# Optimization experiments

Measured on AMD Instinct MI355X. Metric: run time of the kernel, lower is better.

Reference implementation:

```python
import jax, jax.numpy as jnp
import numpy as np

D_STATE = 16
D_CONV = 4


def rmsnorm(x, w, eps=1e-6):
    # normalize over last (channel) axis
    return x * jax.lax.rsqrt(jnp.mean(x * x, axis=-1, keepdims=True) + eps) * w


def silu(x):
    return x * jax.nn.sigmoid(x)


def mamba(x, in_proj_w, conv1d_w, conv1d_b, x_proj_w, dt_proj_w, dt_proj_b, A_log, D_param, out_proj_w):
    # x: [B, L, C], d_inner == C (expand=1)
    B, L, C = x.shape
    dt_rank = dt_proj_w.shape[1]
    xz = jnp.einsum('blc,ec->ble', x, in_proj_w)  # [B, L, 2C]
    u, z = jnp.split(xz, 2, axis=-1)
    # causal depthwise conv1d over time (pad left d_conv-1)
    uc = jax.lax.conv_general_dilated(
        u.transpose(0, 2, 1), conv1d_w[:, None, :], (1,), [(D_CONV - 1, 0)],
        dimension_numbers=('NCH', 'OIH', 'NCH'), feature_group_count=C)
    u = silu((uc + conv1d_b[None, :, None]).transpose(0, 2, 1))  # [B, L, C]
    x_dbl = jnp.einsum('blc,ec->ble', u, x_proj_w)  # [B, L, dt_rank + 2*N]
    dt, Bm, Cm = jnp.split(x_dbl, [dt_rank, dt_rank + D_STATE], axis=-1)
    delta = jax.nn.softplus(jnp.einsum('blr,dr->bld', dt, dt_proj_w) + dt_proj_b)  # [B, L, C]
    A = -jnp.exp(A_log)  # [C, N]
    deltaA = jnp.exp(delta[..., None] * A)              # [B, L, C, N]
    deltaBu = (delta * u)[..., None] * Bm[:, :, None, :]  # [B, L, C, N]

    def step(h, inp):
        dA, dBu, c = inp
        h = dA * h + dBu
        return h, jnp.einsum('bdn,bn->bd', h, c)

    h0 = jnp.zeros((B, C, D_STATE), x.dtype)
    _, ys = jax.lax.scan(step, h0, (deltaA.transpose(1, 0, 2, 3),
                                    deltaBu.transpose(1, 0, 2, 3),
                                    Cm.transpose(1, 0, 2)))
    y = ys.transpose(1, 0, 2) + u * D_param  # [B, L, C]
    y = y * silu(z)
    return jnp.einsum('bld,od->blo', y, out_proj_w)


def reference(x, norm_w, in_proj_w, conv1d_w, conv1d_b, x_proj_w, dt_proj_w, dt_proj_b,
              A_log, D_param, out_proj_w, scale_mod, dw_w, dw_b, res_scale):
    B, C, H, W = x.shape
    x_cl = x.transpose(0, 2, 3, 1)              # [B, H, W, C]
    xn_cl = rmsnorm(x_cl, norm_w)
    x_norm = xn_cl.transpose(0, 3, 1, 2)        # [B, C, H, W]
    # bidirectional Mamba over flattened spatial sequence
    x_flat = xn_cl.reshape(B, H * W, C)
    mparams = (in_proj_w, conv1d_w, conv1d_b, x_proj_w, dt_proj_w, dt_proj_b, A_log, D_param, out_proj_w)
    fwd = mamba(x_flat, *mparams)
    bwd = jnp.flip(mamba(jnp.flip(x_flat, axis=1), *mparams), axis=1)
    g = (fwd + bwd) * scale_mod
    global_feat = g.reshape(B, H, W, C).transpose(0, 3, 1, 2)
    # local spatial gating: sigmoid(depthwise 3x3 conv) * x_norm
    conv = jax.lax.conv_general_dilated(
        x_norm, dw_w[:, None, :, :], (1, 1), [(1, 1), (1, 1)],
        dimension_numbers=('NCHW', 'OIHW', 'NCHW'), feature_group_count=C)
    local_feat = jax.nn.sigmoid(conv + dw_b[None, :, None, None]) * x_norm
    return x + res_scale * (global_feat + local_feat)


def setup_inputs() -> dict:
    key = jax.random.key(0)
    ks = jax.random.split(key, 10)
    B, C, H, W = 8, 384, 32, 32
    dt_rank = 24  # ceil(384 / 16)
    s = 0.02
    f32 = jnp.float32
    return {
        'x': jax.random.normal(ks[0], (B, C, H, W), f32),
        'norm_w': jnp.ones((C,), f32),
        'in_proj_w': jax.random.normal(ks[1], (2 * C, C), f32) * s,
        'conv1d_w': jax.random.normal(ks[2], (C, D_CONV), f32) * 0.2,
        'conv1d_b': jnp.zeros((C,), f32),
        'x_proj_w': jax.random.normal(ks[3], (dt_rank + 2 * D_STATE, C), f32) * s,
        'dt_proj_w': jax.random.normal(ks[4], (C, dt_rank), f32) * 0.1,
        'dt_proj_b': jax.random.uniform(ks[5], (C,), f32, -4.0, -2.0),
        'A_log': jnp.log(jnp.tile(jnp.arange(1, D_STATE + 1, dtype=f32), (C, 1))),
        'D_param': jnp.ones((C,), f32),
        'out_proj_w': jax.random.normal(ks[6], (C, C), f32) * s,
        'scale_mod': jnp.full((1,), 0.25, f32),
        'dw_w': jax.random.normal(ks[7], (C, 3, 3), f32) * 0.1,
        'dw_b': jnp.zeros((C,), f32),
        'res_scale': jnp.full((1,), 0.5, f32),
    }
```

## Files before the change

kernel.cpp:

```cpp
#include <hip/hip_runtime.h>
#include <hip/hip_bf16.h>


typedef __attribute__((ext_vector_type(8))) short bf16x8;
typedef __attribute__((ext_vector_type(8))) unsigned short u16x8;
typedef __attribute__((ext_vector_type(4))) float f32x4;

#define L2E 1.44269504088896340736f

static __device__ __forceinline__ unsigned short f2bf(float f) {
  unsigned int u = __builtin_bit_cast(unsigned int, f);
  u += 0x7fff + ((u >> 16) & 1);
  return (unsigned short)(u >> 16);
}
static __device__ __forceinline__ float bf2f(unsigned short u) {
  unsigned int v = (unsigned int)u << 16;
  return __builtin_bit_cast(float, v);
}

#define GLOAD_LDS16(g, l)                                             \
  __builtin_amdgcn_global_load_lds(                                   \
      (const __attribute__((address_space(1))) unsigned int*)(g),     \
      (__attribute__((address_space(3))) unsigned int*)(l), 16, 0, 0)

__global__ __launch_bounds__(256) void prep_k(
    const float* __restrict__ in_w, const float* __restrict__ x_w,
    const float* __restrict__ dt_w, const float* __restrict__ out_w,
    const float* __restrict__ A_log, const float* __restrict__ nw,
    unsigned short* __restrict__ W_in, unsigned short* __restrict__ W_out,
    unsigned short* __restrict__ Wcomb, float* __restrict__ A2) {
  int idx = blockIdx.x * 256 + threadIdx.x;
  switch (blockIdx.y) {
    case 0: if (idx < 768 * 384) W_in[idx] = f2bf(in_w[idx] * nw[idx % 384]); break;
    case 1: if (idx < 384 * 384) W_out[idx] = f2bf(out_w[idx]); break;
    case 2: if (idx < 384 * 16) A2[idx] = -expf(A_log[idx]) * L2E; break;
    case 3: if (idx < 384 * 384) {
        int o = idx / 384, c = idx - o * 384;
        float s = 0.f;
        #pragma unroll
        for (int r = 0; r < 24; ++r) s += dt_w[o * 24 + r] * x_w[r * 384 + c];
        Wcomb[idx] = f2bf(s);
      } break;
    case 4: if (idx < 128 * 384) {
        int n = idx / 384, k = idx - n * 384;
        Wcomb[147456 + idx] = f2bf(n < 32 ? x_w[(24 + n) * 384 + k] : 0.f);
      } break;
  }
}

__global__ __launch_bounds__(256) void transpose_k(
    const float* __restrict__ x, unsigned short* __restrict__ xb,
    float* __restrict__ nf) {
  const int b = blockIdx.y;
  const int l0 = blockIdx.x * 32;
  const int tid = threadIdx.x;
  const int cr = tid >> 5, lw = tid & 31;
  const int cj = tid & 63, lr = tid >> 6;
  __shared__ float t64[64][33];
  __shared__ float part[8][33];
  float acc = 0.f;
  for (int cc = 0; cc < 6; ++cc) {
    #pragma unroll
    for (int k = 0; k < 8; ++k) {
      int cp = k * 8 + cr;
      int c = cc * 64 + cp;
      float v = x[(((size_t)(b * 384 + c)) << 10) + l0 + lw];
      t64[cp][lw] = v;
      acc = fmaf(v, v, acc);
    }
    __syncthreads();
    #pragma unroll
    for (int k2 = 0; k2 < 8; ++k2) {
      int ll = lr + 4 * k2;
      xb[((size_t)((b << 10) + l0 + ll)) * 384 + cc * 64 + cj] = f2bf(t64[cj][ll]);
    }
    __syncthreads();
  }
  part[cr][lw] = acc;
  __syncthreads();
  if (tid < 32) {
    float s = part[0][tid] + part[1][tid] + part[2][tid] + part[3][tid] +
              part[4][tid] + part[5][tid] + part[6][tid] + part[7][tid];
    nf[(b << 10) + l0 + tid] = rsqrtf(s * (1.f / 384.f) + 1e-6f);
  }
}

template <int EPI, int SUMIN>
__global__ __launch_bounds__(256) void gemm128_k(
    const unsigned short* __restrict__ A0u, const unsigned short* __restrict__ A1u,
    const unsigned short* __restrict__ Bw, int K, int N,
    unsigned short* __restrict__ ob0, unsigned short* __restrict__ ob1,
    float* __restrict__ of0, float* __restrict__ of1,
    const float* __restrict__ aux) {
  const unsigned short* Au = (EPI == 2 && blockIdx.z) ? A1u : A0u;
  unsigned short* ob = (EPI == 2 && blockIdx.z) ? ob1 : ob0;
  float* of = (EPI == 2 && blockIdx.z) ? of1 : of0;
  __shared__ __attribute__((aligned(16))) unsigned short As[128 * 32];
  __shared__ __attribute__((aligned(16))) unsigned short Bs[128 * 32];
  const int n0 = blockIdx.x * 128, m0 = blockIdx.y * 128;
  const int tid = threadIdx.x;
  const int lane = tid & 63, wave = tid >> 6;
  const int wm = wave >> 1, wn = wave & 1;
  const int fr = lane & 15, ks = (lane >> 4) * 8;
  const int row = tid >> 2, colseg = (tid & 3) * 8;
  const unsigned short* pA0 = Au + (size_t)(m0 + row) * K + colseg;
  const unsigned short* pA1 = Au + (size_t)(m0 + 64 + row) * K + colseg;
  const unsigned short* pB0 = Bw + (size_t)(n0 + row) * K + colseg;
  const unsigned short* pB1 = Bw + (size_t)(n0 + 64 + row) * K + colseg;
  unsigned short* lA0 = As + wave * 512;
  unsigned short* lA1 = As + 2048 + wave * 512;
  unsigned short* lB0 = Bs + wave * 512;
  unsigned short* lB1 = Bs + 2048 + wave * 512;
  f32x4 acc[4][4] = {};
  for (int k0 = 0; k0 < K; k0 += 32) {
    __syncthreads();
    if (SUMIN) {
      #pragma unroll
      for (int p = 0; p < 2; ++p) {
        int r = p * 64 + row;
        u16x8 va = *(const u16x8*)&A0u[(size_t)(m0 + r) * K + k0 + colseg];
        u16x8 vb = *(const u16x8*)&A1u[(size_t)(m0 + r) * K + k0 + colseg];
        u16x8 s;
        #pragma unroll
        for (int j = 0; j < 8; ++j) s[j] = f2bf(bf2f(va[j]) + bf2f(vb[j]));
        *(u16x8*)&As[r * 32 + colseg] = s;
      }
    } else {
      GLOAD_LDS16(pA0, lA0);
      GLOAD_LDS16(pA1, lA1);
      pA0 += 32; pA1 += 32;
    }
    GLOAD_LDS16(pB0, lB0);
    GLOAD_LDS16(pB1, lB1);
    pB0 += 32; pB1 += 32;
    __syncthreads();
    bf16x8 af[4], bfr[4];
    #pragma unroll
    for (int mi = 0; mi < 4; ++mi)
      af[mi] = *(const bf16x8*)&As[(wm * 64 + mi * 16 + fr) * 32 + ks];
    #pragma unroll
    for (int ni = 0; ni < 4; ++ni)
      bfr[ni] = *(const bf16x8*)&Bs[(wn * 64 + ni * 16 + fr) * 32 + ks];
    #pragma unroll
    for (int mi = 0; mi < 4; ++mi)
      #pragma unroll
      for (int ni = 0; ni < 4; ++ni)
        acc[mi][ni] = __builtin_amdgcn_mfma_f32_16x16x32_bf16(af[mi], bfr[ni], acc[mi][ni], 0, 0, 0);
  }
  #pragma unroll
  for (int mi = 0; mi < 4; ++mi)
    #pragma unroll
    for (int ni = 0; ni < 4; ++ni)
      #pragma unroll
      for (int j = 0; j < 4; ++j) {
        int m = m0 + wm * 64 + mi * 16 + (lane >> 4) * 4 + j;
        int n = n0 + wn * 64 + ni * 16 + fr;
        float v = acc[mi][ni][j];
        if (EPI == 0) {
          ob0[(size_t)m * N + n] = f2bf(v * aux[m]);
        } else if (EPI == 2) {
          if (n < 384) {
            float t = v + aux[n];
            float sp = (t > 20.f) ? t : log1pf(expf(t));
            ob[(size_t)m * 384 + n] = f2bf(sp);
          } else if (n < 416) {
            of[(size_t)m * 32 + (n - 384)] = v;
          }
        } else {
          ob0[(size_t)m * N + n] = f2bf(v * aux[0]);
        }
      }
}

__global__ __launch_bounds__(384) void conv_silu_k(
    const unsigned short* __restrict__ xz, const float* __restrict__ cw,
    const float* __restrict__ cb,
    unsigned short* __restrict__ ub0, unsigned short* __restrict__ ub1) {
  const int st = blockIdx.x, b = blockIdx.y, dir = blockIdx.z;
  const int c = threadIdx.x;
  const int s0 = st * 8;
  const float w0 = cw[c * 4 + 0], w1 = cw[c * 4 + 1];
  const float w2 = cw[c * 4 + 2], w3 = cw[c * 4 + 3];
  const float bb = cb[c];
  unsigned short* ub = dir ? ub1 : ub0;
  float xv[11];
  #pragma unroll
  for (int k = 0; k < 11; ++k) {
    int j = s0 - 3 + k;
    float v = 0.f;
    if (j >= 0) {
      int t = dir ? (1023 - j) : j;
      v = bf2f(xz[(size_t)((b << 10) + t) * 768 + c]);
    }
    xv[k] = v;
  }
  #pragma unroll
  for (int s = 0; s < 8; ++s) {
    float a = bb + xv[s] * w0 + xv[s + 1] * w1 + xv[s + 2] * w2 + xv[s + 3] * w3;
    float uv = a * __builtin_amdgcn_rcpf(1.f + __builtin_amdgcn_exp2f(-a * L2E));
    ub[(size_t)((b << 10) + s0 + s) * 384 + c] = f2bf(uv);
  }
}

__global__ __launch_bounds__(512) void scan1_k(
    const unsigned short* __restrict__ de0, const unsigned short* __restrict__ de1,
    const unsigned short* __restrict__ ub0, const unsigned short* __restrict__ ub1,
    const float* __restrict__ bc0, const float* __restrict__ bc1,
    const float* __restrict__ A2, float* __restrict__ PH) {
  const int ct = blockIdx.x, b = blockIdx.y;
  const int dir = blockIdx.z >> 4, seg = blockIdx.z & 15;
  const unsigned short* del = dir ? de1 : de0;
  const unsigned short* uu  = dir ? ub1 : ub0;
  const float* bc  = dir ? bc1 : bc0;
  const int tid = threadIdx.x;
  const int lane = tid & 63, wave = tid >> 6;
  const int n = lane & 15, cg = lane >> 4;
  const int cl = wave * 4 + cg;
  const int c = ct * 32 + cl;
  const float a2 = A2[c * 16 + n];
  const size_t base = ((size_t)b << 10) + seg * 64;
  __shared__ __attribute__((aligned(16))) float sd[32][68];
  __shared__ __attribute__((aligned(16))) float su[32][68];
  __shared__ __attribute__((aligned(16))) float sB[16][68];
  const int li = tid >> 5, lj = tid & 31;
  const int li3 = tid >> 4, lj3 = tid & 15;
  unsigned short rd[4], ru[4];
  float rb[2];
  #pragma unroll
  for (int k = 0; k < 4; ++k) {
    size_t rowi = base + k * 16 + li;
    rd[k] = del[rowi * 384 + ct * 32 + lj];
    ru[k] = uu [rowi * 384 + ct * 32 + lj];
  }
  #pragma unroll
  for (int k = 0; k < 2; ++k)
    rb[k] = bc[(base + k * 32 + li3) * 32 + lj3];
  #pragma unroll
  for (int k = 0; k < 4; ++k) {
    float dd = bf2f(rd[k]);
    sd[lj][k * 16 + li] = dd;
    su[lj][k * 16 + li] = dd * bf2f(ru[k]);
  }
  #pragma unroll
  for (int k = 0; k < 2; ++k) sB[lj3][k * 32 + li3] = rb[k];
  __syncthreads();
  float h = 0.f, P = 1.f;
  for (int ch = 0; ch < 4; ++ch) {
    f32x4 dv[4], duv[4], bmv[4];
    #pragma unroll
    for (int r = 0; r < 4; ++r) {
      dv[r]  = *(const f32x4*)&sd[cl][ch * 16 + r * 4];
      duv[r] = *(const f32x4*)&su[cl][ch * 16 + r * 4];
      bmv[r] = *(const f32x4*)&sB[n][ch * 16 + r * 4];
    }
    #pragma unroll
    for (int i = 0; i < 16; ++i) {
      float dA = __builtin_amdgcn_exp2f(dv[i >> 2][i & 3] * a2);
      h = fmaf(dA, h, duv[i >> 2][i & 3] * bmv[i >> 2][i & 3]);
      P *= dA;
    }
  }
  size_t o = (size_t)((dir * 8 + b) * 16 + seg) * 6144 + c * 16 + n;
  *(float2*)&PH[o * 2] = make_float2(P, h);
}

__global__ __launch_bounds__(512) void scan2_k(
    const unsigned short* __restrict__ de0, const unsigned short* __restrict__ de1,
    const unsigned short* __restrict__ ub0, const unsigned short* __restrict__ ub1,
    const float* __restrict__ bc0, const float* __restrict__ bc1,
    const unsigned short* __restrict__ xz, const float* __restrict__ A2,
    const float* __restrict__ Dp, const float* __restrict__ PH,
    unsigned short* __restrict__ Sb0, unsigned short* __restrict__ Sb1) {
  const int ct = blockIdx.x, b = blockIdx.y;
  const int dir = blockIdx.z >> 4, seg = blockIdx.z & 15;
  const unsigned short* del = dir ? de1 : de0;
  const unsigned short* uu  = dir ? ub1 : ub0;
  const float* bc  = dir ? bc1 : bc0;
  unsigned short* S = dir ? Sb1 : Sb0;
  const int tid = threadIdx.x;
  const int lane = tid & 63, wave = tid >> 6;
  const int n = lane & 15, cg = lane >> 4;
  const int cl = wave * 4 + cg;
  const int c = ct * 32 + cl;
  const float a2 = A2[c * 16 + n];
  const float dpc = Dp[c];
  const size_t bb_ = (size_t)b << 10;
  const int segoff = seg * 64;
  __shared__ __attribute__((aligned(16))) float sd[32][68];
  __shared__ __attribute__((aligned(16))) float su[32][68];
  __shared__ __attribute__((aligned(16))) float sz[32][68];
  __shared__ __attribute__((aligned(16))) float sbc[32][68];
  __shared__ __attribute__((aligned(16))) unsigned short sy[64 * 36];
  const int li = tid >> 5, lj = tid & 31;
  unsigned short rd[4], ru[4], rz[4];
  float rb[4];
  #pragma unroll
  for (int k = 0; k < 4; ++k) {
    size_t rowi = bb_ + segoff + k * 16 + li;
    rd[k] = del[rowi * 384 + ct * 32 + lj];
    ru[k] = uu [rowi * 384 + ct * 32 + lj];
    int tz = dir ? (1023 - (segoff + k * 16 + li)) : (segoff + k * 16 + li);
    rz[k] = xz[(bb_ + tz) * 768 + 384 + ct * 32 + lj];
    rb[k] = bc[rowi * 32 + lj];
  }
  float h = 0.f;
  {
    size_t rb2 = (((size_t)(dir * 8 + b) * 16) * 6144 + c * 16 + n) * 2;
    #pragma unroll
    for (int s = 0; s < 15; ++s) {
      float2 ph = *(const float2*)&PH[rb2 + (size_t)s * 12288];
      h = (s < seg) ? fmaf(ph.x, h, ph.y) : h;
    }
  }
  #pragma unroll
  for (int k = 0; k < 4; ++k) {
    sd[lj][k * 16 + li] = bf2f(rd[k]);
    su[lj][k * 16 + li] = bf2f(ru[k]);
    sz[lj][k * 16 + li] = bf2f(rz[k]);
    sbc[lj][k * 16 + li] = rb[k];
  }
  __syncthreads();
  for (int ch = 0; ch < 4; ++ch) {
    f32x4 dv[4], uv4[4], bmv[4], cmv[4];
    #pragma unroll
    for (int r = 0; r < 4; ++r) {
      dv[r]  = *(const f32x4*)&sd[cl][ch * 16 + r * 4];
      uv4[r] = *(const f32x4*)&su[cl][ch * 16 + r * 4];
      bmv[r] = *(const f32x4*)&sbc[n][ch * 16 + r * 4];
      cmv[r] = *(const f32x4*)&sbc[16 + n][ch * 16 + r * 4];
    }
    float p[16];
    #pragma unroll
    for (int i = 0; i < 16; ++i) {
      float dd = dv[i >> 2][i & 3];
      float dA = __builtin_amdgcn_exp2f(dd * a2);
      h = fmaf(dA, h, dd * uv4[i >> 2][i & 3] * bmv[i >> 2][i & 3]);
      p[i] = h * cmv[i >> 2][i & 3];
    }
    float q8[8];
    #pragma unroll
    for (int j = 0; j < 8; ++j) {
      float send = (n & 8) ? p[j] : p[j + 8];
      float recv = __shfl_xor(send, 8);
      float keep = (n & 8) ? p[j + 8] : p[j];
      q8[j] = keep + recv;
    }
    float q4[4];
    #pragma unroll
    for (int j = 0; j < 4; ++j) {
      float send = (n & 4) ? q8[j] : q8[j + 4];
      float recv = __shfl_xor(send, 4);
      float keep = (n & 4) ? q8[j + 4] : q8[j];
      q4[j] = keep + recv;
    }
    float q2[2];
    #pragma unroll
    for (int j = 0; j < 2; ++j) {
      float send = (n & 2) ? q4[j] : q4[j + 2];
      float recv = __shfl_xor(send, 2);
      float keep = (n & 2) ? q4[j + 2] : q4[j];
      q2[j] = keep + recv;
    }
    float send = (n & 1) ? q2[0] : q2[1];
    float recv = __shfl_xor(send, 1);
    float keep = (n & 1) ? q2[1] : q2[0];
    float ysum = keep + recv;
    float uvn = su[cl][ch * 16 + n];
    float zz  = sz[cl][ch * 16 + n];
    float sig = __builtin_amdgcn_rcpf(1.f + __builtin_amdgcn_exp2f(-zz * L2E));
    float y = (ysum + uvn * dpc) * (zz * sig);
    sy[(ch * 16 + n) * 36 + cl] = f2bf(y);
  }
  __syncthreads();
  {
    const int t = tid >> 3, cq = (tid & 7) * 4;
    int tg = segoff + t;
    int trow = dir ? (1023 - tg) : tg;
    *(ushort4*)&S[(bb_ + trow) * 384 + ct * 32 + cq] =
        *(const ushort4*)&sy[t * 36 + cq];
  }
}

__global__ __launch_bounds__(256) void final_k(
    const unsigned short* __restrict__ Gb, const unsigned short* __restrict__ xb,
    const float* __restrict__ nf, const float* __restrict__ nw,
    const float* __restrict__ x, const float* __restrict__ dww,
    const float* __restrict__ dwb, const float* __restrict__ rs,
    float* __restrict__ out) {
  __shared__ float tile[64][33];
  __shared__ float wq[9][64];
  __shared__ float bbs[64], nws[64];
  const int l0 = blockIdx.x * 32, c0 = blockIdx.y * 64, b = blockIdx.z;
  const int tid = threadIdx.x;
  for (int i = tid; i < 576; i += 256) {
    int c = i / 9, q = i - c * 9;
    wq[q][c] = dww[(size_t)(c0 + c) * 9 + q] * nw[c0 + c];
  }
  if (tid < 64) { bbs[tid] = dwb[c0 + tid]; nws[tid] = nw[c0 + tid]; }
  __syncthreads();
  {
    const int oct = tid & 7, li = tid >> 3;
    const int l = l0 + li;
    const int hh = l >> 5, ww = l & 31;
    float acc[8];
    {
      f32x4 ba = *(const f32x4*)&bbs[oct * 8];
      f32x4 bb2 = *(const f32x4*)&bbs[oct * 8 + 4];
      #pragma unroll
      for (int j = 0; j < 4; ++j) { acc[j] = ba[j]; acc[j + 4] = bb2[j]; }
    }
    #pragma unroll
    for (int di = -1; di <= 1; ++di) {
      int h2 = hh + di;
      if (h2 < 0 || h2 > 31) continue;
      #pragma unroll
      for (int dj = -1; dj <= 1; ++dj) {
        int w2 = ww + dj;
        if (w2 < 0 || w2 > 31) continue;
        int lp = h2 * 32 + w2;
        float nfl = nf[(b << 10) + lp];
        u16x8 v = *(const u16x8*)&xb[(size_t)((b << 10) + lp) * 384 + c0 + oct * 8];
        int q = (di + 1) * 3 + (dj + 1);
        f32x4 wa = *(const f32x4*)&wq[q][oct * 8];
        f32x4 wb = *(const f32x4*)&wq[q][oct * 8 + 4];
        #pragma unroll
        for (int j = 0; j < 4; ++j) {
          acc[j]     = fmaf(bf2f(v[j]) * nfl, wa[j], acc[j]);
          acc[j + 4] = fmaf(bf2f(v[j + 4]) * nfl, wb[j], acc[j + 4]);
        }
      }
    }
    size_t ri = (size_t)((b << 10) + l) * 384 + c0 + oct * 8;
    float nfl0 = nf[(b << 10) + l];
    u16x8 xc = *(const u16x8*)&xb[ri];
    u16x8 gv = *(const u16x8*)&Gb[ri];
    #pragma unroll
    for (int j = 0; j < 8; ++j) {
      float xv = bf2f(xc[j]) * nfl0 * nws[oct * 8 + j];
      float sig = __builtin_amdgcn_rcpf(1.f + __builtin_amdgcn_exp2f(-acc[j] * L2E));
      tile[oct * 8 + j][li] = bf2f(gv[j]) + xv * sig;
    }
  }
  __syncthreads();
  {
    const int lw = tid & 31, cr = tid >> 5;
    const float rsv = rs[0];
    for (int p = 0; p < 8; ++p) {
      int c = c0 + p * 8 + cr;
      size_t o = ((size_t)(b * 384 + c) << 10) + l0 + lw;
      out[o] = x[o] + rsv * tile[p * 8 + cr][lw];
    }
  }
}

extern "C" void kernel_launch(void* const* d_in, const int* in_sizes, int n_in,
                              void* d_out, int out_size, void* d_ws, size_t ws_size,
                              hipStream_t stream) {
  const float* x         = (const float*)d_in[0];
  const float* norm_w    = (const float*)d_in[1];
  const float* in_proj_w = (const float*)d_in[2];
  const float* conv1d_w  = (const float*)d_in[3];
  const float* conv1d_b  = (const float*)d_in[4];
  const float* x_proj_w  = (const float*)d_in[5];
  const float* dt_proj_w = (const float*)d_in[6];
  const float* dt_proj_b = (const float*)d_in[7];
  const float* A_log     = (const float*)d_in[8];
  const float* D_param   = (const float*)d_in[9];
  const float* out_proj_w= (const float*)d_in[10];
  const float* scale_mod = (const float*)d_in[11];
  const float* dw_w      = (const float*)d_in[12];
  const float* dw_b      = (const float*)d_in[13];
  const float* res_scale = (const float*)d_in[14];
  float* out = (float*)d_out;

  char* base = (char*)d_ws;
  size_t off = 0;
  auto alloc = [&](size_t bytes) {
    off = (off + 255) & ~(size_t)255;
    void* p = base + off;
    off += bytes;
    return p;
  };
  const size_t B_BLC = (size_t)8192 * 384 * 2;

  unsigned short* xb   = (unsigned short*)alloc(B_BLC);
  float*          nf   = (float*)alloc((size_t)8192 * 4);
  unsigned short* xz   = (unsigned short*)alloc((size_t)8192 * 768 * 2);
  unsigned short* u_b0 = (unsigned short*)alloc(B_BLC);
  unsigned short* u_b1 = (unsigned short*)alloc(B_BLC);
  float*          bc0  = (float*)alloc((size_t)8192 * 32 * 4);
  float*          bc1  = (float*)alloc((size_t)8192 * 32 * 4);
  unsigned short* de0  = (unsigned short*)alloc(B_BLC);
  unsigned short* de1  = (unsigned short*)alloc(B_BLC);
  unsigned short* Sb0  = (unsigned short*)alloc(B_BLC);
  unsigned short* Sb1  = (unsigned short*)alloc(B_BLC);
  float*          PH   = (float*)alloc((size_t)1572864 * 2 * 4);
  unsigned short* W_in = (unsigned short*)alloc((size_t)768 * 384 * 2);
  unsigned short* W_out= (unsigned short*)alloc((size_t)384 * 384 * 2);
  unsigned short* Wcomb= (unsigned short*)alloc((size_t)512 * 384 * 2);
  float*          A2   = (float*)alloc((size_t)384 * 16 * 4);
  unsigned short* Gb   = (unsigned short*)alloc(B_BLC);

  prep_k<<<dim3(1152, 5), 256, 0, stream>>>(in_proj_w, x_proj_w, dt_proj_w,
                                            out_proj_w, A_log, norm_w,
                                            W_in, W_out, Wcomb, A2);
  transpose_k<<<dim3(32, 8), 256, 0, stream>>>(x, xb, nf);
  gemm128_k<0, 0><<<dim3(6, 64), 256, 0, stream>>>(xb, xb, W_in, 384, 768,
                                                   xz, xz, nullptr, nullptr, nf);
  conv_silu_k<<<dim3(128, 8, 2), 384, 0, stream>>>(xz, conv1d_w, conv1d_b,
                                                   u_b0, u_b1);
  gemm128_k<2, 0><<<dim3(4, 64, 2), 256, 0, stream>>>(u_b0, u_b1, Wcomb, 384, 512,
                                                      de0, de1, bc0, bc1,
                                                      dt_proj_b);
  scan1_k<<<dim3(12, 8, 32), 512, 0, stream>>>(de0, de1, u_b0, u_b1, bc0, bc1,
                                               A2, PH);
  scan2_k<<<dim3(12, 8, 32), 512, 0, stream>>>(de0, de1, u_b0, u_b1, bc0, bc1,
                                               xz, A2, D_param, PH, Sb0, Sb1);
  gemm128_k<3, 1><<<dim3(3, 64), 256, 0, stream>>>(Sb0, Sb1, W_out, 384, 384,
                                                   Gb, Gb, nullptr, nullptr,
                                                   scale_mod);
  final_k<<<dim3(32, 6, 8), 256, 0, stream>>>(Gb, xb, nf, norm_w, x, dw_w, dw_b,
                                              res_scale, out);
}
```

Measured before the change: 263.4 us.

## Replace 128x128 GEMM tiles with 64x64 tiles using register-prefetched padded LDS

New measurement: 245.4 us. -6.8%, faster.

```diff
diff --git a/kernel.cpp b/kernel.cpp
--- a/kernel.cpp
+++ b/kernel.cpp
@@ -17,11 +17,6 @@
   unsigned int v = (unsigned int)u << 16;
   return __builtin_bit_cast(float, v);
 }
-
-#define GLOAD_LDS16(g, l)                                             \
-  __builtin_amdgcn_global_load_lds(                                   \
-      (const __attribute__((address_space(1))) unsigned int*)(g),     \
-      (__attribute__((address_space(3))) unsigned int*)(l), 16, 0, 0)
 
 __global__ __launch_bounds__(256) void prep_k(
     const float* __restrict__ in_w, const float* __restrict__ x_w,
@@ -86,75 +81,65 @@
 }
 
 template <int EPI, int SUMIN>
-__global__ __launch_bounds__(256) void gemm128_k(
+__global__ __launch_bounds__(256) void gemm64_k(
     const unsigned short* __restrict__ A0u, const unsigned short* __restrict__ A1u,
     const unsigned short* __restrict__ Bw, int K, int N,
     unsigned short* __restrict__ ob0, unsigned short* __restrict__ ob1,
     float* __restrict__ of0, float* __restrict__ of1,
     const float* __restrict__ aux) {
-  const unsigned short* Au = (EPI == 2 && blockIdx.z) ? A1u : A0u;
-  unsigned short* ob = (EPI == 2 && blockIdx.z) ? ob1 : ob0;
-  float* of = (EPI == 2 && blockIdx.z) ? of1 : of0;
-  __shared__ __attribute__((aligned(16))) unsigned short As[128 * 32];
-  __shared__ __attribute__((aligned(16))) unsigned short Bs[128 * 32];
-  const int n0 = blockIdx.x * 128, m0 = blockIdx.y * 128;
+  const unsigned short* Au = blockIdx.z ? A1u : A0u;
+  unsigned short* ob = blockIdx.z ? ob1 : ob0;
+  float* of = blockIdx.z ? of1 : of0;
+  __shared__ unsigned short As[64][40];
+  __shared__ unsigned short Bs[64][40];
+  const int n0 = blockIdx.x * 64, m0 = blockIdx.y * 64;
   const int tid = threadIdx.x;
   const int lane = tid & 63, wave = tid >> 6;
   const int wm = wave >> 1, wn = wave & 1;
+  const int lrow = tid >> 2, lseg = (tid & 3) * 8;
   const int fr = lane & 15, ks = (lane >> 4) * 8;
-  const int row = tid >> 2, colseg = (tid & 3) * 8;
-  const unsigned short* pA0 = Au + (size_t)(m0 + row) * K + colseg;
-  const unsigned short* pA1 = Au + (size_t)(m0 + 64 + row) * K + colseg;
-  const unsigned short* pB0 = Bw + (size_t)(n0 + row) * K + colseg;
-  const unsigned short* pB1 = Bw + (size_t)(n0 + 64 + row) * K + colseg;
-  unsigned short* lA0 = As + wave * 512;
-  unsigned short* lA1 = As + 2048 + wave * 512;
-  unsigned short* lB0 = Bs + wave * 512;
-  unsigned short* lB1 = Bs + 2048 + wave * 512;
-  f32x4 acc[4][4] = {};
+  const unsigned short* pA = Au + (size_t)(m0 + lrow) * K + lseg;
+  const unsigned short* pA1 = A1u + (size_t)(m0 + lrow) * K + lseg;
+  const unsigned short* pB = Bw + (size_t)(n0 + lrow) * K + lseg;
+  u16x8 rva, rvb, rbb;
+  auto issue = [&](int k0) {
+    rva = *(const u16x8*)(pA + k0);
+    if (SUMIN) rvb = *(const u16x8*)(pA1 + k0);
+    rbb = *(const u16x8*)(pB + k0);
+  };
+  auto commit = [&]() {
+    u16x8 s = rva;
+    if (SUMIN) {
+      #pragma unroll
+      for (int j = 0; j < 8; ++j) s[j] = f2bf(bf2f(rva[j]) + bf2f(rvb[j]));
+    }
+    *(u16x8*)&As[lrow][lseg] = s;
+    *(u16x8*)&Bs[lrow][lseg] = rbb;
+  };
+  issue(0);
+  f32x4 acc[2][2] = {};
   for (int k0 = 0; k0 < K; k0 += 32) {
     __syncthreads();
-    if (SUMIN) {
-      #pragma unroll
-      for (int p = 0; p < 2; ++p) {
-        int r = p * 64 + row;
-        u16x8 va = *(const u16x8*)&A0u[(size_t)(m0 + r) * K + k0 + colseg];
-        u16x8 vb = *(const u16x8*)&A1u[(size_t)(m0 + r) * K + k0 + colseg];
-        u16x8 s;
-        #pragma unroll
-        for (int j = 0; j < 8; ++j) s[j] = f2bf(bf2f(va[j]) + bf2f(vb[j]));
-        *(u16x8*)&As[r * 32 + colseg] = s;
-      }
-    } else {
-      GLOAD_LDS16(pA0, lA0);
-      GLOAD_LDS16(pA1, lA1);
-      pA0 += 32; pA1 += 32;
-    }
-    GLOAD_LDS16(pB0, lB0);
-    GLOAD_LDS16(pB1, lB1);
-    pB0 += 32; pB1 += 32;
+    commit();
     __syncthreads();
-    bf16x8 af[4], bfr[4];
-    #pragma unroll
-    for (int mi = 0; mi < 4; ++mi)
-      af[mi] = *(const bf16x8*)&As[(wm * 64 + mi * 16 + fr) * 32 + ks];
-    #pragma unroll
-    for (int ni = 0; ni < 4; ++ni)
-      bfr[ni] = *(const bf16x8*)&Bs[(wn * 64 + ni * 16 + fr) * 32 + ks];
-    #pragma unroll
-    for (int mi = 0; mi < 4; ++mi)
-      #pragma unroll
-      for (int ni = 0; ni < 4; ++ni)
-        acc[mi][ni] = __builtin_amdgcn_mfma_f32_16x16x32_bf16(af[mi], bfr[ni], acc[mi][ni], 0, 0, 0);
-  }
-  #pragma unroll
-  for (int mi = 0; mi < 4; ++mi)
-    #pragma unroll
-    for (int ni = 0; ni < 4; ++ni)
+    if (k0 + 32 < K) issue(k0 + 32);
+    bf16x8 a0 = *(const bf16x8*)&As[wm * 32 + fr][ks];
+    bf16x8 a1 = *(const bf16x8*)&As[wm * 32 + 16 + fr][ks];
+    bf16x8 b0 = *(const bf16x8*)&Bs[wn * 32 + fr][ks];
+    bf16x8 b1 = *(const bf16x8*)&Bs[wn * 32 + 16 + fr][ks];
+    acc[0][0] = __builtin_amdgcn_mfma_f32_16x16x32_bf16(a0, b0, acc[0][0], 0, 0, 0);
+    acc[0][1] = __builtin_amdgcn_mfma_f32_16x16x32_bf16(a0, b1, acc[0][1], 0, 0, 0);
+    acc[1][0] = __builtin_amdgcn_mfma_f32_16x16x32_bf16(a1, b0, acc[1][0], 0, 0, 0);
+    acc[1][1] = __builtin_amdgcn_mfma_f32_16x16x32_bf16(a1, b1, acc[1][1], 0, 0, 0);
+  }
+  #pragma unroll
+  for (int mi = 0; mi < 2; ++mi)
+    #pragma unroll
+    for (int ni = 0; ni < 2; ++ni)
       #pragma unroll
       for (int j = 0; j < 4; ++j) {
-        int m = m0 + wm * 64 + mi * 16 + (lane >> 4) * 4 + j;
-        int n = n0 + wn * 64 + ni * 16 + fr;
+        int m = m0 + wm * 32 + mi * 16 + (lane >> 4) * 4 + j;
+        int n = n0 + wn * 32 + ni * 16 + (lane & 15);
         float v = acc[mi][ni][j];
         if (EPI == 0) {
           ob0[(size_t)m * N + n] = f2bf(v * aux[m]);
@@ -505,18 +490,18 @@
                                             out_proj_w, A_log, norm_w,
                                             W_in, W_out, Wcomb, A2);
   transpose_k<<<dim3(32, 8), 256, 0, stream>>>(x, xb, nf);
-  gemm128_k<0, 0><<<dim3(6, 64), 256, 0, stream>>>(xb, xb, W_in, 384, 768,
-                                                   xz, xz, nullptr, nullptr, nf);
+  gemm64_k<0, 0><<<dim3(12, 128), 256, 0, stream>>>(xb, xb, W_in, 384, 768,
+                                                    xz, xz, nullptr, nullptr, nf);
   conv_silu_k<<<dim3(128, 8, 2), 384, 0, stream>>>(xz, conv1d_w, conv1d_b,
                                                    u_b0, u_b1);
-  gemm128_k<2, 0><<<dim3(4, 64, 2), 256, 0, stream>>>(u_b0, u_b1, Wcomb, 384, 512,
+  gemm64_k<2, 0><<<dim3(7, 128, 2), 256, 0, stream>>>(u_b0, u_b1, Wcomb, 384, 512,
                                                       de0, de1, bc0, bc1,
                                                       dt_proj_b);
   scan1_k<<<dim3(12, 8, 32), 512, 0, stream>>>(de0, de1, u_b0, u_b1, bc0, bc1,
                                                A2, PH);
   scan2_k<<<dim3(12, 8, 32), 512, 0, stream>>>(de0, de1, u_b0, u_b1, bc0, bc1,
                                                xz, A2, D_param, PH, Sb0, Sb1);
-  gemm128_k<3, 1><<<dim3(3, 64), 256, 0, stream>>>(Sb0, Sb1, W_out, 384, 384,
+  gemm64_k<3, 1><<<dim3(6, 128), 256, 0, stream>>>(Sb0, Sb1, W_out, 384, 384,
                                                    Gb, Gb, nullptr, nullptr,
                                                    scale_mod);
   final_k<<<dim3(32, 6, 8), 256, 0, stream>>>(Gb, xb, nf, norm_w, x, dw_w, dw_b,
```
